# Optimization experiments

Hardware: AMD Instinct MI355X
Metric: run time of the kernel (lower is better)

## Reference

```python
import jax, jax.numpy as jnp
import numpy as np

NEG_SLOPE = 0.2  # PyG GATConv default negative_slope


def _segment_softmax(alpha, dst, n):
    m = jax.ops.segment_max(alpha, dst, num_segments=n)
    m = jnp.where(jnp.isfinite(m), m, 0.0)
    ex = jnp.exp(alpha - m[dst])
    den = jax.ops.segment_sum(ex, dst, num_segments=n)
    return ex / (den[dst] + 1e-16)


def _gat_layer(x, src, dst, eattr, W, att_src, att_dst, We, att_e, b, n):
    h = x @ W                                        # [N, C]
    a = (h @ att_src)[src] + (h @ att_dst)[dst] + (eattr @ We) @ att_e  # [E]
    a = jax.nn.leaky_relu(a, NEG_SLOPE)
    coef = _segment_softmax(a, dst, n)               # edge-wise attention
    out = jax.ops.segment_sum(coef[:, None] * h[src], dst, num_segments=n)
    return out + b


def _glorot(key, shape):
    fan_in, fan_out = shape[0], shape[-1]
    s = jnp.sqrt(6.0 / (fan_in + fan_out))
    return jax.random.uniform(key, shape, jnp.float32, -s, s)


def setup_inputs() -> dict:
    N, E, D, ED = 100000, 1600000, 128, 16
    key = jax.random.key(0)
    ks = jax.random.split(key, 32)
    inp = {
        'x': jax.random.normal(ks[0], (N, D), jnp.float32),
        'edge_index': jax.random.randint(ks[1], (2, E), 0, N, jnp.int64),
        'edge_attr': jax.random.normal(ks[2], (E, ED), jnp.float32),
    }
    dims = [(D, 64), (64, 32), (32, 16)]
    i = 3
    for li, (din, dout) in enumerate(dims, 1):
        inp[f'W{li}'] = _glorot(ks[i], (din, dout)); i += 1
        inp[f'att_src{li}'] = _glorot(ks[i], (dout,)); i += 1
        inp[f'att_dst{li}'] = _glorot(ks[i], (dout,)); i += 1
        inp[f'We{li}'] = _glorot(ks[i], (ED, dout)); i += 1
        inp[f'att_e{li}'] = _glorot(ks[i], (dout,)); i += 1
        inp[f'b{li}'] = jnp.zeros((dout,), jnp.float32)
    return inp


def reference(x, edge_index, edge_attr,
              W1, att_src1, att_dst1, We1, att_e1, b1,
              W2, att_src2, att_dst2, We2, att_e2, b2,
              W3, att_src3, att_dst3, We3, att_e3, b3):
    n = x.shape[0]
    src, dst = edge_index[0], edge_index[1]
    # add self-loops; self-loop edge_attr = mean of incoming edge attrs (fill_value='mean')
    cnt = jax.ops.segment_sum(jnp.ones_like(dst, dtype=edge_attr.dtype), dst, num_segments=n)
    loop_attr = jax.ops.segment_sum(edge_attr, dst, num_segments=n) / jnp.maximum(cnt, 1.0)[:, None]
    loops = jnp.arange(n, dtype=src.dtype)
    src2 = jnp.concatenate([src, loops])
    dst2 = jnp.concatenate([dst, loops])
    ea2 = jnp.concatenate([edge_attr, loop_attr], axis=0)

    h = jax.nn.elu(_gat_layer(x, src2, dst2, ea2, W1, att_src1, att_dst1, We1, att_e1, b1, n))
    h = jax.nn.elu(_gat_layer(h, src2, dst2, ea2, W2, att_src2, att_dst2, We2, att_e2, b2, n))
    z = _gat_layer(h, src2, dst2, ea2, W3, att_src3, att_dst3, We3, att_e3, b3, n)
    return z
```

## Files before the change

kernel.cpp:

```cpp
#include <hip/hip_runtime.h>
#include <hip/hip_bf16.h>

typedef __hip_bfloat16 bf16;

__device__ __forceinline__ float lrelu(float a) { return a > 0.f ? a : 0.2f * a; }
__device__ __forceinline__ int clampi(int v, int hi) { return v < 0 ? 0 : (v >= hi ? hi - 1 : v); }
__device__ __forceinline__ float ldx(const void* p, size_t i, int f32) {
  return f32 ? ((const float*)p)[i] : (float)((const bf16*)p)[i];
}
__device__ __forceinline__ float4 ldx4(const void* p, size_t i, int f32) {
  if (f32) return *(const float4*)((const float*)p + i);
  const __hip_bfloat162* q = (const __hip_bfloat162*)((const bf16*)p + i);
  float2 a = __bfloat1622float2(q[0]), b = __bfloat1622float2(q[1]);
  return make_float4(a.x, a.y, b.x, b.y);
}

__device__ __forceinline__ void edge_qs(const void* eattr, size_t e, int f32, const float* w,
                                        float& q1, float& q2, float& q3) {
  float v[16];
  if (f32) {
    const float4* p = (const float4*)((const float*)eattr + e * 16);
#pragma unroll
    for (int j = 0; j < 4; ++j) {
      float4 t = p[j];
      v[4 * j] = t.x; v[4 * j + 1] = t.y; v[4 * j + 2] = t.z; v[4 * j + 3] = t.w;
    }
  } else {
    const __hip_bfloat162* p = (const __hip_bfloat162*)((const bf16*)eattr + e * 16);
#pragma unroll
    for (int j = 0; j < 8; ++j) {
      float2 t = __bfloat1622float2(p[j]);
      v[2 * j] = t.x; v[2 * j + 1] = t.y;
    }
  }
  q1 = 0.f; q2 = 0.f; q3 = 0.f;
#pragma unroll
  for (int j = 0; j < 16; ++j) {
    q1 += v[j] * w[j];
    q2 += v[j] * w[16 + j];
    q3 += v[j] * w[32 + j];
  }
}

__global__ __launch_bounds__(256) void detect_k(const int* __restrict__ ei32,
                                                const unsigned short* __restrict__ xw, int E,
                                                int* __restrict__ flags) {
  __shared__ int s64, sf;
  int t = threadIdx.x;
  if (t == 0) { s64 = 1; sf = 0; }
  __syncthreads();
  int lim = E < 2048 ? E : 2048;
  for (int k = t; k < lim; k += 256)
    if (ei32[2 * k + 1] != 0) atomicAnd(&s64, 0);
  int hit = 0;
  for (int k = t; k < 4096; k += 256) {
    int ex = (xw[k] >> 7) & 0xFF;
    if (ex >= 0xC3) hit = 1;
  }
  if (hit) atomicOr(&sf, 1);
  __syncthreads();
  if (t == 0) { flags[0] = s64; flags[1] = sf; }
}

__global__ __launch_bounds__(256) void count_k(const int* __restrict__ ei32, int E, int N,
                                               const int* __restrict__ flags,
                                               int* __restrict__ cnt) {
  int is64 = flags[0] != 0;
  int e0 = blockIdx.x * 1024 + threadIdx.x;
#pragma unroll
  for (int i = 0; i < 4; ++i) {
    int e = e0 + i * 256;
    if (e < E) {
      int d = is64 ? ei32[2 * ((size_t)E + e)] : ei32[(size_t)E + e];
      atomicAdd(&cnt[clampi(d, N)], 1);
    }
  }
}

__global__ __launch_bounds__(1024) void scan1_k(const int* __restrict__ cnt, int* __restrict__ excl,
                                                int* __restrict__ bsum, int n) {
  __shared__ int sh[1024];
  int i = blockIdx.x * 1024 + threadIdx.x;
  int v = (i < n) ? cnt[i] : 0;
  sh[threadIdx.x] = v;
  __syncthreads();
  for (int off = 1; off < 1024; off <<= 1) {
    int t = (threadIdx.x >= off) ? sh[threadIdx.x - off] : 0;
    __syncthreads();
    sh[threadIdx.x] += t;
    __syncthreads();
  }
  if (i < n) excl[i] = sh[threadIdx.x] - v;
  if (threadIdx.x == 1023) bsum[blockIdx.x] = sh[1023];
}

__global__ __launch_bounds__(128) void scan2_k(int* bsum, int nb) {
  __shared__ int sh[128];
  int t = threadIdx.x;
  int v = (t < nb) ? bsum[t] : 0;
  sh[t] = v;
  __syncthreads();
  for (int off = 1; off < 128; off <<= 1) {
    int x = (t >= off) ? sh[t - off] : 0;
    __syncthreads();
    sh[t] += x;
    __syncthreads();
  }
  if (t < nb) bsum[t] = sh[t] - v;
}

template <bool FOLD>
__global__ __launch_bounds__(256) void scan3_k(int* __restrict__ row_ptr,
                                               const int* __restrict__ bsum,
                                               int* __restrict__ cur, int n, int E, int nb) {
  __shared__ int pref[128];
  int t = threadIdx.x;
  if (FOLD) {
    if (t < 128) pref[t] = (t < nb) ? bsum[t] : 0;
    __syncthreads();
    for (int off = 1; off < 128; off <<= 1) {
      int x = 0;
      if (t < 128 && t >= off) x = pref[t - off];
      __syncthreads();
      if (t < 128) pref[t] += x;
      __syncthreads();
    }
  }
  int i = blockIdx.x * 256 + t;
  if (i < n) {
    int blk = i >> 10;
    int add = FOLD ? (blk == 0 ? 0 : pref[blk - 1]) : bsum[blk];
    int r = row_ptr[i] + add;
    row_ptr[i] = r;
    cur[i] = r;
  }
  if (i == 0) row_ptr[n] = E;
}

__global__ __launch_bounds__(64) void wvec_k(const void* We1, const void* ae1, const void* We2,
                                             const void* ae2, const void* We3, const void* ae3,
                                             const int* __restrict__ flags, float* wv) {
  int t = threadIdx.x;
  if (t >= 48) return;
  int f32 = flags[1];
  int l = t >> 4, j = t & 15;
  const void* We = l == 0 ? We1 : (l == 1 ? We2 : We3);
  const void* ae = l == 0 ? ae1 : (l == 1 ? ae2 : ae3);
  int C = l == 0 ? 64 : (l == 1 ? 32 : 16);
  float s = 0.f;
  for (int c = 0; c < C; ++c) s += ldx(We, (size_t)j * C + c, f32) * ldx(ae, c, f32);
  wv[l * 16 + j] = s;
}

template <int K, int C, bool XEXT>
__device__ __forceinline__ void mm_body(const void* Xv, const void* Wv, const void* ats_v,
                                        const void* atd_v, int f32, int N, int nblk, float* Wl,
                                        float* Xl, float* __restrict__ h, float* __restrict__ as_,
                                        float* __restrict__ ad_) {
  static_assert(K == 2 * C, "");
  constexpr int NCG = C / 8;
  constexpr int TM = 512 / NCG;
  const int tid = threadIdx.x;
  for (int i = tid; i < K * C; i += 256) Wl[i] = ldx(Wv, i, f32);
  const int cg = tid & (NCG - 1);
  const int ng = tid / NCG;
  const int c0 = cg * 8;
  float ats[8], atd[8];
#pragma unroll
  for (int j = 0; j < 8; ++j) {
    ats[j] = ldx(ats_v, c0 + j, f32);
    atd[j] = ldx(atd_v, c0 + j, f32);
  }
  const int n_base = nblk * TM;
  float acc[2][8];
#pragma unroll
  for (int i = 0; i < 2; ++i)
#pragma unroll
    for (int j = 0; j < 8; ++j) acc[i][j] = 0.f;

#pragma unroll 1
  for (int kc = 0; kc < K / 32; ++kc) {
    __syncthreads();
#pragma unroll
    for (int t = 0; t < TM / 32; ++t) {
      int f = tid + t * 256;
      int node = f >> 3, kq = f & 7;
      int gn = n_base + node;
      if (gn >= N) gn = N - 1;
      float4 v;
      if (XEXT)
        v = ldx4(Xv, (size_t)gn * K + kc * 32 + kq * 4, f32);
      else
        v = *(const float4*)((const float*)Xv + (size_t)gn * K + kc * 32 + kq * 4);
      int col = node ^ (kq * 4);
      Xl[(kq * 4 + 0) * TM + col] = v.x;
      Xl[(kq * 4 + 1) * TM + col] = v.y;
      Xl[(kq * 4 + 2) * TM + col] = v.z;
      Xl[(kq * 4 + 3) * TM + col] = v.w;
    }
    __syncthreads();
#pragma unroll 8
    for (int kk = 0; kk < 32; ++kk) {
      const float2 xv = *(const float2*)&Xl[kk * TM + ((2 * ng) ^ ((kk >> 2) * 4))];
      const float4 w0 = *(const float4*)&Wl[(kc * 32 + kk) * C + c0];
      const float4 w1 = *(const float4*)&Wl[(kc * 32 + kk) * C + c0 + 4];
      const float ws[8] = {w0.x, w0.y, w0.z, w0.w, w1.x, w1.y, w1.z, w1.w};
#pragma unroll
      for (int j = 0; j < 8; ++j) {
        acc[0][j] += xv.x * ws[j];
        acc[1][j] += xv.y * ws[j];
      }
    }
  }
#pragma unroll
  for (int i = 0; i < 2; ++i) {
    int n = n_base + ng * 2 + i;
    float vs = 0.f, vd = 0.f;
#pragma unroll
    for (int j = 0; j < 8; ++j) {
      vs += acc[i][j] * ats[j];
      vd += acc[i][j] * atd[j];
    }
#pragma unroll
    for (int off = NCG / 2; off > 0; off >>= 1) {
      vs += __shfl_xor(vs, off, NCG);
      vd += __shfl_xor(vd, off, NCG);
    }
    if (n < N) {
      float* hr = &h[(size_t)n * C + c0];
      *(float4*)hr = make_float4(acc[i][0], acc[i][1], acc[i][2], acc[i][3]);
      *(float4*)(hr + 4) = make_float4(acc[i][4], acc[i][5], acc[i][6], acc[i][7]);
      if (cg == 0) {
        as_[n] = vs;
        ad_[n] = vd;
      }
    }
  }
}

template <int K, int C, bool XEXT>
__global__ __launch_bounds__(256, 4) void mm3_k(const void* Xv, const void* Wv, const void* ats_v,
                                                const void* atd_v, const int* __restrict__ flags,
                                                int N, float* __restrict__ h,
                                                float* __restrict__ as_, float* __restrict__ ad_) {
  constexpr int TM = 512 / (C / 8);
  __shared__ __align__(16) float Wl[K * C];
  __shared__ __align__(16) float Xl[32 * TM];
  mm_body<K, C, XEXT>(Xv, Wv, ats_v, atd_v, flags[1], N, blockIdx.x, Wl, Xl, h, as_, ad_);
}

template <int K, int C>
__global__ __launch_bounds__(256, 4) void mmscat_k(const void* Xv, const void* Wv,
                                                   const void* ats_v, const void* atd_v,
                                                   const int* __restrict__ flags, int N,
                                                   float* __restrict__ h, float* __restrict__ as_,
                                                   float* __restrict__ ad_, int MMG,
                                                   const int* __restrict__ ei32, const void* eattr,
                                                   const float* __restrict__ wv,
                                                   int* __restrict__ cur,
                                                   float4* __restrict__ recs, int E) {
  constexpr int TM = 512 / (C / 8);
  __shared__ __align__(16) float Wl[K * C];
  __shared__ __align__(16) float Xl[32 * TM];
  if ((int)blockIdx.x >= MMG) {
    if (threadIdx.x < 48) Wl[threadIdx.x] = wv[threadIdx.x];
    __syncthreads();
    int chunk = blockIdx.x - MMG;
    int is64 = flags[0] != 0, f32 = flags[1] != 0;
    int e0 = chunk * 1024 + threadIdx.x;
    int ss[4], dd[4], valid[4];
    float q1[4], q2[4], q3[4];
#pragma unroll
    for (int i = 0; i < 4; ++i) {
      int e = e0 + i * 256;
      valid[i] = e < E;
      ss[i] = 0; dd[i] = 0;
      if (valid[i]) {
        int s = is64 ? ei32[2 * (size_t)e] : ei32[e];
        int d = is64 ? ei32[2 * ((size_t)E + e)] : ei32[(size_t)E + e];
        ss[i] = clampi(s, N);
        dd[i] = clampi(d, N);
      }
    }
#pragma unroll
    for (int i = 0; i < 4; ++i)
      if (valid[i]) edge_qs(eattr, (size_t)(e0 + i * 256), f32, Wl, q1[i], q2[i], q3[i]);
    int pos[4];
#pragma unroll
    for (int i = 0; i < 4; ++i)
      if (valid[i]) pos[i] = atomicAdd(&cur[dd[i]], 1);
#pragma unroll
    for (int i = 0; i < 4; ++i)
      if (valid[i])
        recs[clampi(pos[i], E)] = make_float4(__int_as_float(ss[i]), q1[i], q2[i], q3[i]);
    return;
  }
  mm_body<K, C, true>(Xv, Wv, ats_v, atd_v, flags[1], N, blockIdx.x, Wl, Xl, h, as_, ad_);
}

template <int C, int QC, bool ELU, bool LAST>
__global__ __launch_bounds__(256) void agg_k(const int* __restrict__ row_ptr,
                                             const float4* __restrict__ recs,
                                             const float* __restrict__ as_,
                                             const float* __restrict__ ad_,
                                             const float* __restrict__ h, const void* b,
                                             const int* __restrict__ flags, void* out, int N,
                                             int E) {
  const int GR = 256 / C;
  __shared__ int ss[256];
  __shared__ float sp[256];
  int lane = threadIdx.x & (C - 1);
  int grp = threadIdx.x / C;
  int slot0 = grp * C;
  int f32 = flags[1];
  float bc = ldx(b, lane, f32);
  for (int n = blockIdx.x * GR + grp; n < N; n += gridDim.x * GR) {
    int start = row_ptr[n], end = row_ptr[n + 1];
    int deg = end > start ? end - start : 0;
    float qsum = 0.f;
    for (int j = lane; j < deg; j += C) {
      float4 r = recs[start + j];
      qsum += ((const float*)&r)[QC];
    }
#pragma unroll
    for (int off = C / 2; off > 0; off >>= 1) qsum += __shfl_xor(qsum, off, C);
    float qloop = qsum / fmaxf((float)deg, 1.0f);
    float adn = ad_[n];
    float m = lrelu(as_[n] + adn + qloop), den = 1.0f;
    float acc = h[(size_t)n * C + lane];
    for (int base = 0; base < deg; base += C) {
      int cnt = deg - base < C ? deg - base : C;
      int sj = 0;
      float aj = -1e30f;
      if (lane < cnt) {
        float4 r = recs[start + base + lane];
        sj = clampi(__float_as_int(r.x), N);
        aj = lrelu(as_[sj] + adn + ((const float*)&r)[QC]);
      }
      float cm = aj;
#pragma unroll
      for (int off = C / 2; off > 0; off >>= 1) cm = fmaxf(cm, __shfl_xor(cm, off, C));
      float nm = fmaxf(m, cm);
      float sc = __expf(m - nm);
      float pj = (lane < cnt) ? __expf(aj - nm) : 0.f;
      float ps = pj;
#pragma unroll
      for (int off = C / 2; off > 0; off >>= 1) ps += __shfl_xor(ps, off, C);
      den = den * sc + ps;
      m = nm;
      ss[slot0 + lane] = sj;
      sp[slot0 + lane] = pj;
      float accs = 0.f;
#pragma unroll 8
      for (int jj = 0; jj < cnt; ++jj) {
        int s = ss[slot0 + jj];
        float p = sp[slot0 + jj];
        accs += p * h[(size_t)s * C + lane];
      }
      acc = acc * sc + accs;
    }
    float o = acc / (den + 1e-16f) + bc;
    if (ELU) o = o > 0.f ? o : (__expf(o) - 1.0f);
    if (LAST && !f32)
      ((bf16*)out)[(size_t)n * C + lane] = (bf16)o;
    else
      ((float*)out)[(size_t)n * C + lane] = o;
  }
}

extern "C" void kernel_launch(void* const* d_in, const int* in_sizes, int n_in, void* d_out,
                              int out_size, void* d_ws, size_t ws_size, hipStream_t stream) {
  const void* x = d_in[0];
  const int* ei32 = (const int*)d_in[1];
  void* eattr = d_in[2];
  const void *W1 = d_in[3], *s1 = d_in[4], *t1 = d_in[5], *We1 = d_in[6], *ae1 = d_in[7],
             *b1 = d_in[8];
  const void *W2 = d_in[9], *s2 = d_in[10], *t2 = d_in[11], *We2 = d_in[12], *ae2 = d_in[13],
             *b2 = d_in[14];
  const void *W3 = d_in[15], *s3 = d_in[16], *t3 = d_in[17], *We3 = d_in[18], *ae3 = d_in[19],
             *b3 = d_in[20];

  const int N = in_sizes[0] / 128;
  const int E = in_sizes[1] / 2;

  char* p = (char*)d_ws;
  auto alloc = [&](size_t bytes) -> void* {
    void* r = (void*)p;
    p += (bytes + 255) & ~(size_t)255;
    return r;
  };
  int* row_ptr = (int*)alloc((size_t)(N + 1) * 4);
  float4* recs = (float4*)alloc((size_t)E * 16);
  int* cnt = (int*)alloc((size_t)N * 4);
  int* cur = (int*)alloc((size_t)N * 4);
  int* bsum = (int*)alloc(128 * 4);
  float* wv = (float*)alloc(64 * 4);
  int* flags = (int*)alloc(256);
  float* as_ = (float*)alloc((size_t)N * 4);
  float* ad_ = (float*)alloc((size_t)N * 4);
  size_t used = (size_t)(p - (char*)d_ws);
  size_t need = 2 * ((size_t)N * 64 * 4 + 256);
  float *bufH, *bufO;
  if (used + need <= ws_size) {
    bufH = (float*)alloc((size_t)N * 64 * 4);
    bufO = (float*)alloc((size_t)N * 64 * 4);
  } else {
    bufH = (float*)eattr;
    bufO = (float*)eattr + (size_t)N * 64;
  }

  hipMemsetAsync(cnt, 0, (size_t)N * 4, stream);
  detect_k<<<1, 256, 0, stream>>>(ei32, (const unsigned short*)x, E, flags);
  wvec_k<<<1, 64, 0, stream>>>(We1, ae1, We2, ae2, We3, ae3, flags, wv);
  count_k<<<(E + 1023) / 1024, 256, 0, stream>>>(ei32, E, N, flags, cnt);
  int nb = (N + 1023) / 1024;
  scan1_k<<<nb, 1024, 0, stream>>>(cnt, row_ptr, bsum, N);
  if (nb <= 128) {
    scan3_k<true><<<(N + 255) / 256, 256, 0, stream>>>(row_ptr, bsum, cur, N, E, nb);
  } else {
    scan2_k<<<1, 128, 0, stream>>>(bsum, nb);
    scan3_k<false><<<(N + 255) / 256, 256, 0, stream>>>(row_ptr, bsum, cur, N, E, nb);
  }

  int MMG = (N + 63) / 64;
  int SCG = (E + 1023) / 1024;
  mmscat_k<128, 64><<<MMG + SCG, 256, 0, stream>>>(x, W1, s1, t1, flags, N, bufH, as_, ad_, MMG,
                                                   ei32, eattr, wv, cur, recs, E);
  agg_k<64, 1, true, false><<<(N + 3) / 4, 256, 0, stream>>>(row_ptr, recs, as_, ad_, bufH, b1,
                                                             flags, bufO, N, E);
  mm3_k<64, 32, false><<<(N + 127) / 128, 256, 0, stream>>>(bufO, W2, s2, t2, flags, N, bufH, as_,
                                                            ad_);
  agg_k<32, 2, true, false><<<(N + 7) / 8, 256, 0, stream>>>(row_ptr, recs, as_, ad_, bufH, b2,
                                                             flags, bufO, N, E);
  mm3_k<32, 16, false><<<(N + 255) / 256, 256, 0, stream>>>(bufO, W3, s3, t3, flags, N, bufH, as_,
                                                            ad_);
  agg_k<16, 3, false, true><<<(N + 15) / 16, 256, 0, stream>>>(row_ptr, recs, as_, ad_, bufH, b3,
                                                               flags, d_out, N, E);
}
```

Before: 595.7 us.

## Split fused matmul/scatter kernel, merge detect with wvec, fold self-loop into online softmax

Splits the combined layer-1 matmul and edge-scatter kernel back into a separate scatter kernel and a plain matmul kernel. The flag-detection and edge-weight-vector kernels are merged into one launch. The aggregation kernel no longer makes a separate pass over the edge records to compute the self-loop attribute mean. It accumulates that sum during the main online-softmax loop and adds the self-loop term at the end, which removes one read of the records per node. In exchange, the matmul and scatter no longer run concurrently within a single launch, and one extra kernel launch is added.

```diff
diff --git a/kernel.cpp b/kernel.cpp
--- a/kernel.cpp
+++ b/kernel.cpp
@@ -42,9 +42,12 @@
   }
 }
 
-__global__ __launch_bounds__(256) void detect_k(const int* __restrict__ ei32,
-                                                const unsigned short* __restrict__ xw, int E,
-                                                int* __restrict__ flags) {
+__global__ __launch_bounds__(256) void detwv_k(const int* __restrict__ ei32,
+                                               const unsigned short* __restrict__ xw, int E,
+                                               int* __restrict__ flags, const void* We1,
+                                               const void* ae1, const void* We2, const void* ae2,
+                                               const void* We3, const void* ae3,
+                                               float* __restrict__ wv) {
   __shared__ int s64, sf;
   int t = threadIdx.x;
   if (t == 0) { s64 = 1; sf = 0; }
@@ -60,6 +63,16 @@
   if (hit) atomicOr(&sf, 1);
   __syncthreads();
   if (t == 0) { flags[0] = s64; flags[1] = sf; }
+  int f32 = sf;
+  if (t < 48) {
+    int l = t >> 4, j = t & 15;
+    const void* We = l == 0 ? We1 : (l == 1 ? We2 : We3);
+    const void* ae = l == 0 ? ae1 : (l == 1 ? ae2 : ae3);
+    int Cc = l == 0 ? 64 : (l == 1 ? 32 : 16);
+    float s = 0.f;
+    for (int c = 0; c < Cc; ++c) s += ldx(We, (size_t)j * Cc + c, f32) * ldx(ae, c, f32);
+    wv[l * 16 + j] = s;
+  }
 }
 
 __global__ __launch_bounds__(256) void count_k(const int* __restrict__ ei32, int E, int N,
@@ -137,29 +150,53 @@
   if (i == 0) row_ptr[n] = E;
 }
 
-__global__ __launch_bounds__(64) void wvec_k(const void* We1, const void* ae1, const void* We2,
-                                             const void* ae2, const void* We3, const void* ae3,
-                                             const int* __restrict__ flags, float* wv) {
-  int t = threadIdx.x;
-  if (t >= 48) return;
-  int f32 = flags[1];
-  int l = t >> 4, j = t & 15;
-  const void* We = l == 0 ? We1 : (l == 1 ? We2 : We3);
-  const void* ae = l == 0 ? ae1 : (l == 1 ? ae2 : ae3);
-  int C = l == 0 ? 64 : (l == 1 ? 32 : 16);
-  float s = 0.f;
-  for (int c = 0; c < C; ++c) s += ldx(We, (size_t)j * C + c, f32) * ldx(ae, c, f32);
-  wv[l * 16 + j] = s;
+__global__ __launch_bounds__(256) void scatter_k(const int* __restrict__ ei32, const void* eattr,
+                                                 const float* __restrict__ wv,
+                                                 const int* __restrict__ flags,
+                                                 int* __restrict__ cur,
+                                                 float4* __restrict__ recs, int E, int N) {
+  __shared__ float w[48];
+  if (threadIdx.x < 48) w[threadIdx.x] = wv[threadIdx.x];
+  __syncthreads();
+  int is64 = flags[0] != 0, f32 = flags[1] != 0;
+  int e0 = blockIdx.x * 1024 + threadIdx.x;
+  int ss[4], dd[4], valid[4];
+  float q1[4], q2[4], q3[4];
+#pragma unroll
+  for (int i = 0; i < 4; ++i) {
+    int e = e0 + i * 256;
+    valid[i] = e < E;
+    ss[i] = 0; dd[i] = 0;
+    if (valid[i]) {
+      int s = is64 ? ei32[2 * (size_t)e] : ei32[e];
+      int d = is64 ? ei32[2 * ((size_t)E + e)] : ei32[(size_t)E + e];
+      ss[i] = clampi(s, N);
+      dd[i] = clampi(d, N);
+    }
+  }
+#pragma unroll
+  for (int i = 0; i < 4; ++i)
+    if (valid[i]) edge_qs(eattr, (size_t)(e0 + i * 256), f32, w, q1[i], q2[i], q3[i]);
+  int pos[4];
+#pragma unroll
+  for (int i = 0; i < 4; ++i)
+    if (valid[i]) pos[i] = atomicAdd(&cur[dd[i]], 1);
+#pragma unroll
+  for (int i = 0; i < 4; ++i)
+    if (valid[i]) recs[clampi(pos[i], E)] = make_float4(__int_as_float(ss[i]), q1[i], q2[i], q3[i]);
 }
 
 template <int K, int C, bool XEXT>
-__device__ __forceinline__ void mm_body(const void* Xv, const void* Wv, const void* ats_v,
-                                        const void* atd_v, int f32, int N, int nblk, float* Wl,
-                                        float* Xl, float* __restrict__ h, float* __restrict__ as_,
-                                        float* __restrict__ ad_) {
+__global__ __launch_bounds__(256, 4) void mm3_k(const void* Xv, const void* Wv, const void* ats_v,
+                                                const void* atd_v, const int* __restrict__ flags,
+                                                int N, float* __restrict__ h,
+                                                float* __restrict__ as_, float* __restrict__ ad_) {
   static_assert(K == 2 * C, "");
   constexpr int NCG = C / 8;
   constexpr int TM = 512 / NCG;
+  __shared__ __align__(16) float Wl[K * C];
+  __shared__ __align__(16) float Xl[32 * TM];
+  const int f32 = flags[1];
   const int tid = threadIdx.x;
   for (int i = tid; i < K * C; i += 256) Wl[i] = ldx(Wv, i, f32);
   const int cg = tid & (NCG - 1);
@@ -171,7 +208,7 @@
     ats[j] = ldx(ats_v, c0 + j, f32);
     atd[j] = ldx(atd_v, c0 + j, f32);
   }
-  const int n_base = nblk * TM;
+  const int n_base = blockIdx.x * TM;
   float acc[2][8];
 #pragma unroll
   for (int i = 0; i < 2; ++i)
@@ -236,66 +273,6 @@
       }
     }
   }
-}
-
-template <int K, int C, bool XEXT>
-__global__ __launch_bounds__(256, 4) void mm3_k(const void* Xv, const void* Wv, const void* ats_v,
-                                                const void* atd_v, const int* __restrict__ flags,
-                                                int N, float* __restrict__ h,
-                                                float* __restrict__ as_, float* __restrict__ ad_) {
-  constexpr int TM = 512 / (C / 8);
-  __shared__ __align__(16) float Wl[K * C];
-  __shared__ __align__(16) float Xl[32 * TM];
-  mm_body<K, C, XEXT>(Xv, Wv, ats_v, atd_v, flags[1], N, blockIdx.x, Wl, Xl, h, as_, ad_);
-}
-
-template <int K, int C>
-__global__ __launch_bounds__(256, 4) void mmscat_k(const void* Xv, const void* Wv,
-                                                   const void* ats_v, const void* atd_v,
-                                                   const int* __restrict__ flags, int N,
-                                                   float* __restrict__ h, float* __restrict__ as_,
-                                                   float* __restrict__ ad_, int MMG,
-                                                   const int* __restrict__ ei32, const void* eattr,
-                                                   const float* __restrict__ wv,
-                                                   int* __restrict__ cur,
-                                                   float4* __restrict__ recs, int E) {
-  constexpr int TM = 512 / (C / 8);
-  __shared__ __align__(16) float Wl[K * C];
-  __shared__ __align__(16) float Xl[32 * TM];
-  if ((int)blockIdx.x >= MMG) {
-    if (threadIdx.x < 48) Wl[threadIdx.x] = wv[threadIdx.x];
-    __syncthreads();
-    int chunk = blockIdx.x - MMG;
-    int is64 = flags[0] != 0, f32 = flags[1] != 0;
-    int e0 = chunk * 1024 + threadIdx.x;
-    int ss[4], dd[4], valid[4];
-    float q1[4], q2[4], q3[4];
-#pragma unroll
-    for (int i = 0; i < 4; ++i) {
-      int e = e0 + i * 256;
-      valid[i] = e < E;
-      ss[i] = 0; dd[i] = 0;
-      if (valid[i]) {
-        int s = is64 ? ei32[2 * (size_t)e] : ei32[e];
-        int d = is64 ? ei32[2 * ((size_t)E + e)] : ei32[(size_t)E + e];
-        ss[i] = clampi(s, N);
-        dd[i] = clampi(d, N);
-      }
-    }
-#pragma unroll
-    for (int i = 0; i < 4; ++i)
-      if (valid[i]) edge_qs(eattr, (size_t)(e0 + i * 256), f32, Wl, q1[i], q2[i], q3[i]);
-    int pos[4];
-#pragma unroll
-    for (int i = 0; i < 4; ++i)
-      if (valid[i]) pos[i] = atomicAdd(&cur[dd[i]], 1);
-#pragma unroll
-    for (int i = 0; i < 4; ++i)
-      if (valid[i])
-        recs[clampi(pos[i], E)] = make_float4(__int_as_float(ss[i]), q1[i], q2[i], q3[i]);
-    return;
-  }
-  mm_body<K, C, true>(Xv, Wv, ats_v, atd_v, flags[1], N, blockIdx.x, Wl, Xl, h, as_, ad_);
 }
 
 template <int C, int QC, bool ELU, bool LAST>
@@ -317,26 +294,19 @@
   for (int n = blockIdx.x * GR + grp; n < N; n += gridDim.x * GR) {
     int start = row_ptr[n], end = row_ptr[n + 1];
     int deg = end > start ? end - start : 0;
-    float qsum = 0.f;
-    for (int j = lane; j < deg; j += C) {
-      float4 r = recs[start + j];
-      qsum += ((const float*)&r)[QC];
-    }
-#pragma unroll
-    for (int off = C / 2; off > 0; off >>= 1) qsum += __shfl_xor(qsum, off, C);
-    float qloop = qsum / fmaxf((float)deg, 1.0f);
     float adn = ad_[n];
-    float m = lrelu(as_[n] + adn + qloop), den = 1.0f;
-    float acc = h[(size_t)n * C + lane];
+    float m = -1e30f, den = 0.f, acc = 0.f, qacc = 0.f;
     for (int base = 0; base < deg; base += C) {
       int cnt = deg - base < C ? deg - base : C;
       int sj = 0;
-      float aj = -1e30f;
+      float aj = -1e30f, qv = 0.f;
       if (lane < cnt) {
         float4 r = recs[start + base + lane];
         sj = clampi(__float_as_int(r.x), N);
-        aj = lrelu(as_[sj] + adn + ((const float*)&r)[QC]);
+        qv = ((const float*)&r)[QC];
+        aj = lrelu(as_[sj] + adn + qv);
       }
+      qacc += qv;
       float cm = aj;
 #pragma unroll
       for (int off = C / 2; off > 0; off >>= 1) cm = fmaxf(cm, __shfl_xor(cm, off, C));
@@ -359,6 +329,16 @@
       }
       acc = acc * sc + accs;
     }
+    float qsum = qacc;
+#pragma unroll
+    for (int off = C / 2; off > 0; off >>= 1) qsum += __shfl_xor(qsum, off, C);
+    float qloop = qsum / fmaxf((float)deg, 1.0f);
+    float aself = lrelu(as_[n] + adn + qloop);
+    float nm = fmaxf(m, aself);
+    float sc = __expf(m - nm);
+    float pself = __expf(aself - nm);
+    den = den * sc + pself;
+    acc = acc * sc + pself * h[(size_t)n * C + lane];
     float o = acc / (den + 1e-16f) + bc;
     if (ELU) o = o > 0.f ? o : (__expf(o) - 1.0f);
     if (LAST && !f32)
@@ -410,8 +390,8 @@
   }
 
   hipMemsetAsync(cnt, 0, (size_t)N * 4, stream);
-  detect_k<<<1, 256, 0, stream>>>(ei32, (const unsigned short*)x, E, flags);
-  wvec_k<<<1, 64, 0, stream>>>(We1, ae1, We2, ae2, We3, ae3, flags, wv);
+  detwv_k<<<1, 256, 0, stream>>>(ei32, (const unsigned short*)x, E, flags, We1, ae1, We2, ae2, We3,
+                                 ae3, wv);
   count_k<<<(E + 1023) / 1024, 256, 0, stream>>>(ei32, E, N, flags, cnt);
   int nb = (N + 1023) / 1024;
   scan1_k<<<nb, 1024, 0, stream>>>(cnt, row_ptr, bsum, N);
@@ -421,11 +401,9 @@
     scan2_k<<<1, 128, 0, stream>>>(bsum, nb);
     scan3_k<false><<<(N + 255) / 256, 256, 0, stream>>>(row_ptr, bsum, cur, N, E, nb);
   }
-
-  int MMG = (N + 63) / 64;
-  int SCG = (E + 1023) / 1024;
-  mmscat_k<128, 64><<<MMG + SCG, 256, 0, stream>>>(x, W1, s1, t1, flags, N, bufH, as_, ad_, MMG,
-                                                   ei32, eattr, wv, cur, recs, E);
+  scatter_k<<<(E + 1023) / 1024, 256, 0, stream>>>(ei32, eattr, wv, flags, cur, recs, E, N);
+
+  mm3_k<128, 64, true><<<(N + 63) / 64, 256, 0, stream>>>(x, W1, s1, t1, flags, N, bufH, as_, ad_);
   agg_k<64, 1, true, false><<<(N + 3) / 4, 256, 0, stream>>>(row_ptr, recs, as_, ad_, bufH, b1,
                                                              flags, bufO, N, E);
   mm3_k<64, 32, false><<<(N + 127) / 128, 256, 0, stream>>>(bufO, W2, s2, t2, flags, N, bufH, as_,
```

Result: no change. 602.7 us (+1.2%).
